# Performance work log

Hardware: AMD Instinct MI355X
Metric: run time of the kernel (lower is better)

Reference implementation:

```python
import jax, jax.numpy as jnp
import numpy as np

VOCAB = 32000
HIDDEN = 1024


def setup_inputs() -> dict:
    key = jax.random.key(0)
    k1, k2, k3 = jax.random.split(key, 3)
    inputs = jax.random.randint(k1, (4, 4096), 0, VOCAB, dtype=jnp.int64 if jax.config.jax_enable_x64 else jnp.int32)
    W0 = jax.random.normal(k2, (VOCAB, 2 * HIDDEN), dtype=jnp.float32)
    W1 = jax.random.normal(k3, (2 * HIDDEN, HIDDEN), dtype=jnp.float32)
    return {"inputs": inputs, "W0": W0, "W1": W1}


def reference(inputs, W0, W1):
    # Original builds one-hot [N, V] and does two GEMMs; mathematically this is
    # a gather of W0 rows followed by a matmul with W1.
    x = W0[inputs]                      # [B, L, 2H]  (== one_hot @ W0)
    emb = jnp.einsum('blk,kh->blh', x, W1)  # [B, L, H]
    mask = (inputs != 0).astype(emb.dtype)  # zero out padding token 0
    emb = emb * mask[..., None]
    emb = emb * jnp.asarray(HIDDEN ** 0.5, emb.dtype)
    return emb
```

## Files before the change

### kernel.cpp

```cpp
#include <hip/hip_runtime.h>
#include <stdint.h>

#define VOCAB 32000
#define KDIM  2048
#define NDIM  1024
#define MTOK  16384

typedef __bf16 bf16x8 __attribute__((ext_vector_type(8)));
typedef float  f32x4  __attribute__((ext_vector_type(4)));

__device__ __forceinline__ uint32_t pkbf(float a, float b) {
    union { __bf16 h[2]; uint32_t u; } r;
    r.h[0] = (__bf16)a; r.h[1] = (__bf16)b;
    return r.u;
}

__device__ __forceinline__ unsigned short f2bf(float f) {
    union { float f; uint32_t u; } v; v.f = f;
    uint32_t u = v.u;
    return (unsigned short)((u + 0x7FFFu + ((u >> 16) & 1u)) >> 16);
}

__device__ __forceinline__ void gload_lds16(const void* g, void* l) {
    __builtin_amdgcn_global_load_lds(
        (const __attribute__((address_space(1))) uint32_t*)g,
        (__attribute__((address_space(3))) uint32_t*)l,
        16, 0, 0);
}

__global__ void w1_transpose_kernel(const float* __restrict__ W1,
                                    unsigned short* __restrict__ W1T) {
    __shared__ unsigned short tile[32][33];
    const int k0 = blockIdx.x * 32;
    const int n0 = blockIdx.y * 32;
    const int tx = threadIdx.x;
    const int ty = threadIdx.y;
#pragma unroll
    for (int i = 0; i < 4; ++i) {
        int kl = ty + i * 8;
        tile[kl][tx] = __builtin_bit_cast(unsigned short,
                            (__bf16)W1[(size_t)(k0 + kl) * NDIM + n0 + tx]);
    }
    __syncthreads();
#pragma unroll
    for (int i = 0; i < 4; ++i) {
        int nl = ty + i * 8;
        W1T[(size_t)(n0 + nl) * KDIM + k0 + tx] = tile[tx][nl];
    }
}

__global__ __launch_bounds__(512, 2)
void emb_gemm_ws(const int* __restrict__ idx,
                 const float* __restrict__ W0,
                 const unsigned short* __restrict__ W1T,
                 float* __restrict__ out) {
    __shared__ __align__(16) char Abuf[2][256 * 128];
    __shared__ __align__(16) char Bbuf[2][256 * 128];

    const int tid  = threadIdx.x;
    const int lane = tid & 63;
    const int wav  = tid >> 6;
    const int wm   = wav >> 2;
    const int wn   = wav & 3;
    const int m0   = blockIdx.x * 256;
    const int n0   = blockIdx.y * 256;

    const int ac = tid & 15;
    uint32_t aoff[8];
    int abyte[8];
#pragma unroll
    for (int it = 0; it < 8; ++it) {
        const int r = (tid >> 4) + it * 32;
        aoff[it]  = ((uint32_t)idx[m0 + r] * KDIM + ac * 4) * 4u;
        abyte[it] = (r * 128 + ac * 8) ^ ((r & 7) << 4);
    }

    const int brin = lane >> 3;
    const int bch  = (lane & 7) ^ brin;
    uint32_t boff[4];
    int bbase[4];
#pragma unroll
    for (int i = 0; i < 4; ++i) {
        const int rg = wav * 32 + i * 8;
        boff[i]  = ((uint32_t)(n0 + rg + brin) * KDIM + bch * 8) * 2u;
        bbase[i] = rg * 128;
    }

    f32x4 apre[4];
    f32x4 acc[8][4] = {};
    bf16x8 af[4], bf2[4], bfv[4];

    const int rl = lane & 15;
    const int kq = (lane >> 4) * 16;

#define ISSUE_A_H(t, h)                                              \
    _Pragma("unroll")                                                \
    for (int j = 0; j < 4; ++j)                                      \
        apre[j] = *(const f32x4*)((const char*)W0 + aoff[(h) * 4 + j] + (t) * 256);

#define WRITE_A_H(buf, h)                                            \
    _Pragma("unroll")                                                \
    for (int j = 0; j < 4; ++j) {                                    \
        uint2 pk;                                                    \
        pk.x = pkbf(apre[j][0], apre[j][1]);                         \
        pk.y = pkbf(apre[j][2], apre[j][3]);                         \
        *(uint2*)(Abuf[buf] + abyte[(h) * 4 + j]) = pk;              \
    }

#define ISSUE_B(buf, t)                                              \
    _Pragma("unroll")                                                \
    for (int i = 0; i < 4; ++i)                                      \
        gload_lds16((const char*)W1T + boff[i] + (t) * 128,          \
                    Bbuf[buf] + bbase[i]);

#define READ_A(buf, ks, mh, dst)                                     \
    _Pragma("unroll")                                                \
    for (int mi = 0; mi < 4; ++mi) {                                 \
        const int r = wm * 128 + (mh) * 64 + mi * 16 + rl;           \
        dst[mi] = *(const bf16x8*)(Abuf[buf] +                       \
            ((r * 128 + (ks) * 64 + kq) ^ ((r & 7) << 4)));          \
    }

#define READ_B(buf, ks, dst)                                         \
    _Pragma("unroll")                                                \
    for (int ni = 0; ni < 4; ++ni) {                                 \
        const int n = wn * 64 + ni * 16 + rl;                        \
        dst[ni] = *(const bf16x8*)(Bbuf[buf] +                       \
            ((n * 128 + (ks) * 64 + kq) ^ ((n & 7) << 4)));          \
    }

#define MFMA16(a_, b_, mh)                                           \
    __builtin_amdgcn_s_setprio(1);                                   \
    _Pragma("unroll")                                                \
    for (int mi = 0; mi < 4; ++mi)                                   \
        _Pragma("unroll")                                            \
        for (int ni = 0; ni < 4; ++ni)                               \
            acc[(mh) * 4 + mi][ni] =                                 \
                __builtin_amdgcn_mfma_f32_16x16x32_bf16(             \
                    a_[mi], b_[ni], acc[(mh) * 4 + mi][ni], 0, 0, 0);\
    __builtin_amdgcn_s_setprio(0);

    ISSUE_B(0, 0);
    ISSUE_A_H(0, 0); WRITE_A_H(0, 0);
    ISSUE_A_H(0, 1); WRITE_A_H(0, 1);
    __syncthreads();

    for (int t = 0; t < 32; ++t) {
        const int cur = t & 1, nxt = cur ^ 1;
        const bool pf = (t < 31);

        if (pf) { ISSUE_B(nxt, t + 1); ISSUE_A_H(t + 1, 0); }

        READ_B(cur, 0, bfv);
        READ_A(cur, 0, 0, af);
        MFMA16(af, bfv, 0);
        READ_A(cur, 0, 1, af);
        MFMA16(af, bfv, 1);

        if (pf) { WRITE_A_H(nxt, 0); ISSUE_A_H(t + 1, 1); }

        READ_B(cur, 1, bf2);
        READ_A(cur, 1, 0, af);
        MFMA16(af, bf2, 0);
        READ_A(cur, 1, 1, af);
        MFMA16(af, bf2, 1);

        if (pf) { WRITE_A_H(nxt, 1); }
        __syncthreads();
    }

    const int rowq = (lane >> 4) * 4;
#pragma unroll
    for (int mi = 0; mi < 8; ++mi) {
#pragma unroll
        for (int r = 0; r < 4; ++r) {
            const int m = m0 + wm * 128 + mi * 16 + rowq + r;
            const float msk = (idx[m] != 0) ? 32.0f : 0.0f;
#pragma unroll
            for (int ni = 0; ni < 4; ++ni) {
                const int n = n0 + wn * 64 + ni * 16 + rl;
                out[(size_t)m * NDIM + n] = acc[mi][ni][r] * msk;
            }
        }
    }
#undef ISSUE_A_H
#undef WRITE_A_H
#undef ISSUE_B
#undef READ_A
#undef READ_B
#undef MFMA16
}

__global__ __launch_bounds__(256)
void emb_gemm_nows(const int* __restrict__ idx,
                   const float* __restrict__ W0,
                   const float* __restrict__ W1,
                   float* __restrict__ out) {
    __shared__ __align__(16) char A_lds[128 * 128];
    __shared__ __align__(16) char B_lds[128 * 128];

    const int tid  = threadIdx.x;
    const int lane = tid & 63;
    const int wav  = tid >> 6;
    const int wm = wav >> 1;
    const int wn = wav & 1;
    const int m0 = blockIdx.x * 128;
    const int n0 = blockIdx.y * 128;

    const float* aSrc[8];
    int arow[8];
#pragma unroll
    for (int it = 0; it < 8; ++it) {
        int r = it * 16 + (tid >> 4);
        arow[it] = r;
        aSrc[it] = W0 + (size_t)idx[m0 + r] * KDIM;
    }
    const int acol4 = tid & 15;

    f32x4 acc[4][4] = {};

    for (int k0 = 0; k0 < KDIM; k0 += 64) {
#pragma unroll
        for (int it = 0; it < 8; ++it) {
            const int r = arow[it];
            const float4 v = *(const float4*)(aSrc[it] + k0 + acol4 * 4);
            uint2 pk;
            pk.x = pkbf(v.x, v.y);
            pk.y = pkbf(v.z, v.w);
            *(uint2*)(A_lds + ((r * 128 + acol4 * 8) ^ ((r & 7) << 4))) = pk;
        }
#pragma unroll
        for (int it = 0; it < 8; ++it) {
            const int k  = it * 8 + (tid >> 5);
            const int n4 = (tid & 31) * 4;
            const float4 v = *(const float4*)(W1 + (size_t)(k0 + k) * NDIM + n0 + n4);
            unsigned short h[4] = { f2bf(v.x), f2bf(v.y), f2bf(v.z), f2bf(v.w) };
#pragma unroll
            for (int i = 0; i < 4; ++i) {
                const int n = n4 + i;
                *(unsigned short*)(B_lds + ((n * 128 + k * 2) ^ ((n & 7) << 4))) = h[i];
            }
        }
        __syncthreads();

#pragma unroll
        for (int ks = 0; ks < 2; ++ks) {
            const int kb = ks * 64 + (lane >> 4) * 16;
            bf16x8 af[4], bfv[4];
#pragma unroll
            for (int mi = 0; mi < 4; ++mi) {
                const int r = wm * 64 + mi * 16 + (lane & 15);
                af[mi] = *(const bf16x8*)(A_lds + ((r * 128 + kb) ^ ((r & 7) << 4)));
            }
#pragma unroll
            for (int ni = 0; ni < 4; ++ni) {
                const int n = wn * 64 + ni * 16 + (lane & 15);
                bfv[ni] = *(const bf16x8*)(B_lds + ((n * 128 + kb) ^ ((n & 7) << 4)));
            }
#pragma unroll
            for (int mi = 0; mi < 4; ++mi)
#pragma unroll
                for (int ni = 0; ni < 4; ++ni)
                    acc[mi][ni] = __builtin_amdgcn_mfma_f32_16x16x32_bf16(
                        af[mi], bfv[ni], acc[mi][ni], 0, 0, 0);
        }
        __syncthreads();
    }

    const int col  = lane & 15;
    const int rowq = (lane >> 4) * 4;
#pragma unroll
    for (int mi = 0; mi < 4; ++mi) {
#pragma unroll
        for (int r = 0; r < 4; ++r) {
            const int m = m0 + wm * 64 + mi * 16 + rowq + r;
            const float msk = (idx[m] != 0) ? 32.0f : 0.0f;
#pragma unroll
            for (int ni = 0; ni < 4; ++ni) {
                const int n = n0 + wn * 64 + ni * 16 + col;
                out[(size_t)m * NDIM + n] = acc[mi][ni][r] * msk;
            }
        }
    }
}

extern "C" void kernel_launch(void* const* d_in, const int* in_sizes, int n_in,
                              void* d_out, int out_size, void* d_ws, size_t ws_size,
                              hipStream_t stream) {
    const int*   idx = (const int*)d_in[0];
    const float* W0  = (const float*)d_in[1];
    const float* W1  = (const float*)d_in[2];
    float*       out = (float*)d_out;

    const size_t w1t_bytes = (size_t)KDIM * NDIM * 2;

    if (ws_size >= w1t_bytes) {
        unsigned short* W1T = (unsigned short*)d_ws;
        dim3 tgrid(KDIM / 32, NDIM / 32);
        w1_transpose_kernel<<<tgrid, dim3(32, 8), 0, stream>>>(W1, W1T);
        dim3 grid(MTOK / 256, NDIM / 256);
        emb_gemm_ws<<<grid, 512, 0, stream>>>(idx, W0, W1T, out);
    } else {
        dim3 grid(MTOK / 128, NDIM / 128);
        emb_gemm_nows<<<grid, 256, 0, stream>>>(idx, W0, W1, out);
    }
}
```

Baseline: 89.30 us.

## Load B operand fragments directly from global into registers, dropping B LDS buffer

The W1T tile no longer goes through LDS via global_load_lds. Each wave now loads its bf16x8 B fragments straight from global memory into registers, double-buffered across the two k-halves. This halves LDS use per block and removes the B-side LDS reads, which may improve occupancy. In exchange, B data is no longer shared across the two M-waves, so global/L2 traffic for B rises and load latency is exposed closer to the MFMAs.

```diff
diff --git a/kernel.cpp b/kernel.cpp
--- a/kernel.cpp
+++ b/kernel.cpp
@@ -19,13 +19,6 @@
     union { float f; uint32_t u; } v; v.f = f;
     uint32_t u = v.u;
     return (unsigned short)((u + 0x7FFFu + ((u >> 16) & 1u)) >> 16);
-}
-
-__device__ __forceinline__ void gload_lds16(const void* g, void* l) {
-    __builtin_amdgcn_global_load_lds(
-        (const __attribute__((address_space(1))) uint32_t*)g,
-        (__attribute__((address_space(3))) uint32_t*)l,
-        16, 0, 0);
 }
 
 __global__ void w1_transpose_kernel(const float* __restrict__ W1,
@@ -55,7 +48,6 @@
                  const unsigned short* __restrict__ W1T,
                  float* __restrict__ out) {
     __shared__ __align__(16) char Abuf[2][256 * 128];
-    __shared__ __align__(16) char Bbuf[2][256 * 128];
 
     const int tid  = threadIdx.x;
     const int lane = tid & 63;
@@ -65,6 +57,9 @@
     const int m0   = blockIdx.x * 256;
     const int n0   = blockIdx.y * 256;
 
+    const int rl = lane & 15;
+    const int kg = (lane >> 4) * 16;
+
     const int ac = tid & 15;
     uint32_t aoff[8];
     int abyte[8];
@@ -75,23 +70,14 @@
         abyte[it] = (r * 128 + ac * 8) ^ ((r & 7) << 4);
     }
 
-    const int brin = lane >> 3;
-    const int bch  = (lane & 7) ^ brin;
-    uint32_t boff[4];
-    int bbase[4];
-#pragma unroll
-    for (int i = 0; i < 4; ++i) {
-        const int rg = wav * 32 + i * 8;
-        boff[i]  = ((uint32_t)(n0 + rg + brin) * KDIM + bch * 8) * 2u;
-        bbase[i] = rg * 128;
-    }
+    uint32_t bcol[4];
+#pragma unroll
+    for (int ni = 0; ni < 4; ++ni)
+        bcol[ni] = ((uint32_t)(n0 + wn * 64 + ni * 16 + rl) * KDIM) * 2u + kg;
 
     f32x4 apre[4];
     f32x4 acc[8][4] = {};
-    bf16x8 af[4], bf2[4], bfv[4];
-
-    const int rl = lane & 15;
-    const int kq = (lane >> 4) * 16;
+    bf16x8 bA[4], bB[4], af[4];
 
 #define ISSUE_A_H(t, h)                                              \
     _Pragma("unroll")                                                \
@@ -101,32 +87,24 @@
 #define WRITE_A_H(buf, h)                                            \
     _Pragma("unroll")                                                \
     for (int j = 0; j < 4; ++j) {                                    \
-        uint2 pk;                                                    \
-        pk.x = pkbf(apre[j][0], apre[j][1]);                         \
-        pk.y = pkbf(apre[j][2], apre[j][3]);                         \
-        *(uint2*)(Abuf[buf] + abyte[(h) * 4 + j]) = pk;              \
-    }
-
-#define ISSUE_B(buf, t)                                              \
-    _Pragma("unroll")                                                \
-    for (int i = 0; i < 4; ++i)                                      \
-        gload_lds16((const char*)W1T + boff[i] + (t) * 128,          \
-                    Bbuf[buf] + bbase[i]);
+        uint2 pk_;                                                   \
+        pk_.x = pkbf(apre[j][0], apre[j][1]);                        \
+        pk_.y = pkbf(apre[j][2], apre[j][3]);                        \
+        *(uint2*)(Abuf[buf] + abyte[(h) * 4 + j]) = pk_;             \
+    }
+
+#define ISSUE_B(dst, t, ks)                                          \
+    _Pragma("unroll")                                                \
+    for (int ni = 0; ni < 4; ++ni)                                   \
+        dst[ni] = *(const bf16x8*)((const char*)W1T + bcol[ni] +     \
+                                   (t) * 128 + (ks) * 64);
 
 #define READ_A(buf, ks, mh, dst)                                     \
     _Pragma("unroll")                                                \
     for (int mi = 0; mi < 4; ++mi) {                                 \
         const int r = wm * 128 + (mh) * 64 + mi * 16 + rl;           \
         dst[mi] = *(const bf16x8*)(Abuf[buf] +                       \
-            ((r * 128 + (ks) * 64 + kq) ^ ((r & 7) << 4)));          \
-    }
-
-#define READ_B(buf, ks, dst)                                         \
-    _Pragma("unroll")                                                \
-    for (int ni = 0; ni < 4; ++ni) {                                 \
-        const int n = wn * 64 + ni * 16 + rl;                        \
-        dst[ni] = *(const bf16x8*)(Bbuf[buf] +                       \
-            ((n * 128 + (ks) * 64 + kq) ^ ((n & 7) << 4)));          \
+            ((r * 128 + (ks) * 64 + kg) ^ ((r & 7) << 4)));          \
     }
 
 #define MFMA16(a_, b_, mh)                                           \
@@ -140,7 +118,8 @@
                     a_[mi], b_[ni], acc[(mh) * 4 + mi][ni], 0, 0, 0);\
     __builtin_amdgcn_s_setprio(0);
 
-    ISSUE_B(0, 0);
+    ISSUE_B(bA, 0, 0);
+    ISSUE_B(bB, 0, 1);
     ISSUE_A_H(0, 0); WRITE_A_H(0, 0);
     ISSUE_A_H(0, 1); WRITE_A_H(0, 1);
     __syncthreads();
@@ -149,23 +128,28 @@
         const int cur = t & 1, nxt = cur ^ 1;
         const bool pf = (t < 31);
 
-        if (pf) { ISSUE_B(nxt, t + 1); ISSUE_A_H(t + 1, 0); }
-
-        READ_B(cur, 0, bfv);
+        if (pf) { ISSUE_A_H(t + 1, 0); }
+
         READ_A(cur, 0, 0, af);
-        MFMA16(af, bfv, 0);
+        MFMA16(af, bA, 0);
         READ_A(cur, 0, 1, af);
-        MFMA16(af, bfv, 1);
-
-        if (pf) { WRITE_A_H(nxt, 0); ISSUE_A_H(t + 1, 1); }
-
-        READ_B(cur, 1, bf2);
+        MFMA16(af, bA, 1);
+
+        if (pf) {
+            ISSUE_B(bA, t + 1, 0);
+            WRITE_A_H(nxt, 0);
+            ISSUE_A_H(t + 1, 1);
+        }
+
         READ_A(cur, 1, 0, af);
-        MFMA16(af, bf2, 0);
+        MFMA16(af, bB, 0);
         READ_A(cur, 1, 1, af);
-        MFMA16(af, bf2, 1);
-
-        if (pf) { WRITE_A_H(nxt, 1); }
+        MFMA16(af, bB, 1);
+
+        if (pf) {
+            ISSUE_B(bB, t + 1, 1);
+            WRITE_A_H(nxt, 1);
+        }
         __syncthreads();
     }
 
@@ -187,7 +171,6 @@
 #undef WRITE_A_H
 #undef ISSUE_B
 #undef READ_A
-#undef READ_B
 #undef MFMA16
 }
 
```

Result: slower. 95.90 us (+7.4%).

## Shrink workspace GEMM tile to 128x128 with 4 waves and prefetch fragments

Applied to the files above, without the earlier changes.

The gather-GEMM block tile drops from 256x256 with 8 waves to 128x128 with 4 waves, and the grid grows to match, so more blocks are available to spread across CUs. Each wave now loads both k-halves of its A and B fragments from LDS before issuing its MFMAs, instead of interleaving reads with compute. The cost is that each gathered W0 row and each W1T tile is fetched by twice as many blocks, which raises global and L2 traffic on the fp32 embedding gather.

```diff
diff --git a/kernel.cpp b/kernel.cpp
--- a/kernel.cpp
+++ b/kernel.cpp
@@ -49,28 +49,31 @@
     }
 }
 
-__global__ __launch_bounds__(512, 2)
+__global__ __launch_bounds__(256, 2)
 void emb_gemm_ws(const int* __restrict__ idx,
                  const float* __restrict__ W0,
                  const unsigned short* __restrict__ W1T,
                  float* __restrict__ out) {
-    __shared__ __align__(16) char Abuf[2][256 * 128];
-    __shared__ __align__(16) char Bbuf[2][256 * 128];
+    __shared__ __align__(16) char Abuf[2][128 * 128];
+    __shared__ __align__(16) char Bbuf[2][128 * 128];
 
     const int tid  = threadIdx.x;
     const int lane = tid & 63;
     const int wav  = tid >> 6;
-    const int wm   = wav >> 2;
-    const int wn   = wav & 3;
-    const int m0   = blockIdx.x * 256;
-    const int n0   = blockIdx.y * 256;
+    const int wm   = wav >> 1;
+    const int wn   = wav & 1;
+    const int m0   = blockIdx.x * 128;
+    const int n0   = blockIdx.y * 128;
+
+    const int rl = lane & 15;
+    const int kg = (lane >> 4) * 16;
 
     const int ac = tid & 15;
     uint32_t aoff[8];
     int abyte[8];
 #pragma unroll
     for (int it = 0; it < 8; ++it) {
-        const int r = (tid >> 4) + it * 32;
+        const int r = (tid >> 4) + it * 16;
         aoff[it]  = ((uint32_t)idx[m0 + r] * KDIM + ac * 4) * 4u;
         abyte[it] = (r * 128 + ac * 8) ^ ((r & 7) << 4);
     }
@@ -87,11 +90,8 @@
     }
 
     f32x4 apre[4];
-    f32x4 acc[8][4] = {};
-    bf16x8 af[4], bf2[4], bfv[4];
-
-    const int rl = lane & 15;
-    const int kq = (lane >> 4) * 16;
+    f32x4 acc[4][4] = {};
+    bf16x8 afX[4], afY[4], bfX[4], bfY[4];
 
 #define ISSUE_A_H(t, h)                                              \
     _Pragma("unroll")                                                \
@@ -101,24 +101,24 @@
 #define WRITE_A_H(buf, h)                                            \
     _Pragma("unroll")                                                \
     for (int j = 0; j < 4; ++j) {                                    \
-        uint2 pk;                                                    \
-        pk.x = pkbf(apre[j][0], apre[j][1]);                         \
-        pk.y = pkbf(apre[j][2], apre[j][3]);                         \
-        *(uint2*)(Abuf[buf] + abyte[(h) * 4 + j]) = pk;              \
-    }
-
-#define ISSUE_B(buf, t)                                              \
+        uint2 pk_;                                                   \
+        pk_.x = pkbf(apre[j][0], apre[j][1]);                        \
+        pk_.y = pkbf(apre[j][2], apre[j][3]);                        \
+        *(uint2*)(Abuf[buf] + abyte[(h) * 4 + j]) = pk_;             \
+    }
+
+#define DMA_B(buf, t)                                                \
     _Pragma("unroll")                                                \
     for (int i = 0; i < 4; ++i)                                      \
         gload_lds16((const char*)W1T + boff[i] + (t) * 128,          \
                     Bbuf[buf] + bbase[i]);
 
-#define READ_A(buf, ks, mh, dst)                                     \
+#define READ_A(buf, ks, dst)                                         \
     _Pragma("unroll")                                                \
     for (int mi = 0; mi < 4; ++mi) {                                 \
-        const int r = wm * 128 + (mh) * 64 + mi * 16 + rl;           \
+        const int r = wm * 64 + mi * 16 + rl;                        \
         dst[mi] = *(const bf16x8*)(Abuf[buf] +                       \
-            ((r * 128 + (ks) * 64 + kq) ^ ((r & 7) << 4)));          \
+            ((r * 128 + (ks) * 64 + kg) ^ ((r & 7) << 4)));          \
     }
 
 #define READ_B(buf, ks, dst)                                         \
@@ -126,21 +126,20 @@
     for (int ni = 0; ni < 4; ++ni) {                                 \
         const int n = wn * 64 + ni * 16 + rl;                        \
         dst[ni] = *(const bf16x8*)(Bbuf[buf] +                       \
-            ((n * 128 + (ks) * 64 + kq) ^ ((n & 7) << 4)));          \
-    }
-
-#define MFMA16(a_, b_, mh)                                           \
+            ((n * 128 + (ks) * 64 + kg) ^ ((n & 7) << 4)));          \
+    }
+
+#define MFMA16(a_, b_)                                               \
     __builtin_amdgcn_s_setprio(1);                                   \
     _Pragma("unroll")                                                \
     for (int mi = 0; mi < 4; ++mi)                                   \
         _Pragma("unroll")                                            \
         for (int ni = 0; ni < 4; ++ni)                               \
-            acc[(mh) * 4 + mi][ni] =                                 \
-                __builtin_amdgcn_mfma_f32_16x16x32_bf16(             \
-                    a_[mi], b_[ni], acc[(mh) * 4 + mi][ni], 0, 0, 0);\
+            acc[mi][ni] = __builtin_amdgcn_mfma_f32_16x16x32_bf16(   \
+                a_[mi], b_[ni], acc[mi][ni], 0, 0, 0);               \
     __builtin_amdgcn_s_setprio(0);
 
-    ISSUE_B(0, 0);
+    DMA_B(0, 0);
     ISSUE_A_H(0, 0); WRITE_A_H(0, 0);
     ISSUE_A_H(0, 1); WRITE_A_H(0, 1);
     __syncthreads();
@@ -149,21 +148,16 @@
         const int cur = t & 1, nxt = cur ^ 1;
         const bool pf = (t < 31);
 
-        if (pf) { ISSUE_B(nxt, t + 1); ISSUE_A_H(t + 1, 0); }
-
-        READ_B(cur, 0, bfv);
-        READ_A(cur, 0, 0, af);
-        MFMA16(af, bfv, 0);
-        READ_A(cur, 0, 1, af);
-        MFMA16(af, bfv, 1);
+        if (pf) { DMA_B(nxt, t + 1); ISSUE_A_H(t + 1, 0); }
+
+        READ_A(cur, 0, afX); READ_B(cur, 0, bfX);
+        READ_A(cur, 1, afY); READ_B(cur, 1, bfY);
+
+        MFMA16(afX, bfX);
 
         if (pf) { WRITE_A_H(nxt, 0); ISSUE_A_H(t + 1, 1); }
 
-        READ_B(cur, 1, bf2);
-        READ_A(cur, 1, 0, af);
-        MFMA16(af, bf2, 0);
-        READ_A(cur, 1, 1, af);
-        MFMA16(af, bf2, 1);
+        MFMA16(afY, bfY);
 
         if (pf) { WRITE_A_H(nxt, 1); }
         __syncthreads();
@@ -171,10 +165,10 @@
 
     const int rowq = (lane >> 4) * 4;
 #pragma unroll
-    for (int mi = 0; mi < 8; ++mi) {
+    for (int mi = 0; mi < 4; ++mi) {
 #pragma unroll
         for (int r = 0; r < 4; ++r) {
-            const int m = m0 + wm * 128 + mi * 16 + rowq + r;
+            const int m = m0 + wm * 64 + mi * 16 + rowq + r;
             const float msk = (idx[m] != 0) ? 32.0f : 0.0f;
 #pragma unroll
             for (int ni = 0; ni < 4; ++ni) {
@@ -185,7 +179,7 @@
     }
 #undef ISSUE_A_H
 #undef WRITE_A_H
-#undef ISSUE_B
+#undef DMA_B
 #undef READ_A
 #undef READ_B
 #undef MFMA16
@@ -298,8 +292,8 @@
         unsigned short* W1T = (unsigned short*)d_ws;
         dim3 tgrid(KDIM / 32, NDIM / 32);
         w1_transpose_kernel<<<tgrid, dim3(32, 8), 0, stream>>>(W1, W1T);
-        dim3 grid(MTOK / 256, NDIM / 256);
-        emb_gemm_ws<<<grid, 512, 0, stream>>>(idx, W0, W1T, out);
+        dim3 grid(MTOK / 128, NDIM / 128);
+        emb_gemm_ws<<<grid, 256, 0, stream>>>(idx, W0, W1T, out);
     } else {
         dim3 grid(MTOK / 128, NDIM / 128);
         emb_gemm_nows<<<grid, 256, 0, stream>>>(idx, W0, W1, out);
```

Result: slower. 106.1 us (+18.8%).
